# Kernel tuning notes

Measured on AMD Instinct MI355X. Metric: run time of the kernel, lower is better.

## Reference

```python
import math
import jax, jax.numpy as jnp
import numpy as np

B, S, D, QK, H = 4, 4096, 1024, 128, 2048  # hidden = int(2.0 * dim)
NUM_BUCKETS, MAX_DIST = 32, 128
LN_EPS = 1e-5


def setup_inputs() -> dict:
    key = jax.random.key(0)
    ks = jax.random.split(key, 7)
    x = jax.random.normal(ks[0], (B, S, D), jnp.float32)
    ln_g = jnp.ones((D,), jnp.float32)
    ln_b = jnp.zeros((D,), jnp.float32)
    Wh = jax.random.normal(ks[1], (D, 2 * H), jnp.float32) * 0.02
    bh = jnp.zeros((2 * H,), jnp.float32)
    Wqk = jax.random.normal(ks[2], (D, QK), jnp.float32) * 0.02
    bqk = jnp.zeros((QK,), jnp.float32)
    os_gamma = jax.random.normal(ks[3], (2, QK), jnp.float32) * 0.02  # nn.init.normal_(std=0.02)
    os_beta = jnp.zeros((2, QK), jnp.float32)
    Wo = jax.random.normal(ks[4], (H, D), jnp.float32) * 0.02
    bo = jnp.zeros((D,), jnp.float32)
    rel_emb = jax.random.normal(ks[5], (NUM_BUCKETS, 1), jnp.float32) * 0.02
    return {"x": x, "ln_g": ln_g, "ln_b": ln_b, "Wh": Wh, "bh": bh,
            "Wqk": Wqk, "bqk": bqk, "os_gamma": os_gamma, "os_beta": os_beta,
            "Wo": Wo, "bo": bo, "rel_emb": rel_emb}


def _t5_rel_bias(rel_emb, seq_len, scale):
    # non-causal T5 relative position bucket (num_buckets halved to 16)
    pos = jnp.arange(seq_len)
    rel = pos[None, :] - pos[:, None]  # k_pos - q_pos -> [i, j]
    n = -rel
    nb = NUM_BUCKETS // 2  # 16
    me = nb // 2           # max_exact = 8
    ret = (n < 0).astype(jnp.int32) * nb
    na = jnp.abs(n)
    val_large = me + (jnp.log(jnp.maximum(na, 1).astype(jnp.float32) / me)
                      / math.log(MAX_DIST / me) * (nb - me)).astype(jnp.int32)
    val_large = jnp.minimum(val_large, nb - 1)
    bucket = ret + jnp.where(na < me, na, val_large)  # [S, S] in [0, 31]
    return rel_emb[bucket, 0] * scale  # [S, S]


def reference(x, ln_g, ln_b, Wh, bh, Wqk, bqk, os_gamma, os_beta, Wo, bo, rel_emb):
    seq_len = x.shape[-2]
    # LayerNorm
    mu = jnp.mean(x, axis=-1, keepdims=True)
    var = jnp.mean(jnp.square(x - mu), axis=-1, keepdims=True)
    normed = (x - mu) * jax.lax.rsqrt(var + LN_EPS) * ln_g + ln_b
    # hidden (v, gate) with SiLU
    hidden = jax.nn.silu(normed @ Wh + bh)  # [B, S, 2H]
    v, gate = hidden[..., :H], hidden[..., H:]
    # qk projection + offset/scale into q, k
    qk = jax.nn.silu(normed @ Wqk + bqk)  # [B, S, QK]
    q = qk * os_gamma[0] + os_beta[0]
    k = qk * os_gamma[1] + os_beta[1]
    sim = jnp.einsum('bid,bjd->bij', q, k)  # [B, S, S]
    sim = sim + _t5_rel_bias(rel_emb, seq_len, float(D) ** 0.5)
    attn = jnp.square(jax.nn.relu(sim / seq_len))  # ReLU^2, no softmax
    out = jnp.einsum('bij,bjd->bid', attn, v) * gate  # [B, S, H]
    out = out @ Wo + bo
    return out + x  # add_residual
```

## Files before the change

kernel.cpp:

```cpp
#include <hip/hip_runtime.h>
#include <hip/hip_bf16.h>
#include <math.h>

typedef __bf16 bf16_t;
typedef __bf16 bf16x8 __attribute__((ext_vector_type(8)));
typedef __bf16 bf16x4 __attribute__((ext_vector_type(4)));
typedef float  f32x4  __attribute__((ext_vector_type(4)));
typedef int    i32x4  __attribute__((ext_vector_type(4)));

#define S_LEN 4096
#define D_DIM 1024
#define QK_DIM 128
#define H_DIM 2048
#define BATCH 4

__device__ __forceinline__ void gld_lds16(const void* g, void* l) {
  __builtin_amdgcn_global_load_lds((const __attribute__((address_space(1))) void*)g,
                                   (__attribute__((address_space(3))) void*)l, 16, 0, 0);
}

__device__ __forceinline__ float silu_f(float v) {
  return v / (1.0f + __expf(-v));
}

__device__ __forceinline__ bf16x8 as_bf(i32x4 v) {
  union { i32x4 a; bf16x8 b; } u; u.a = v; return u.b;
}

__device__ __forceinline__ float ldf(const void* p, size_t i, int f32) {
  return f32 ? ((const float*)p)[i] : (float)((const bf16_t*)p)[i];
}

__global__ void probe_k(const unsigned* __restrict__ ln_g_raw, int* __restrict__ flag) {
  if (threadIdx.x == 0) flag[0] = (ln_g_raw[0] == 0x3F800000u) ? 1 : 0;
}

#define M_HID 0
#define M_QK 1
#define M_SCORE 2
#define M_PV 3
#define M_OUT 4

template <int MODE, int K, int WAVES>
__global__ __launch_bounds__(WAVES * 64, 4)
void gemm2b(const bf16_t* __restrict__ A, const bf16_t* __restrict__ Bt,
            const void* e0, const void* e1, const float* __restrict__ ef,
            void* o0, void* o1, const int* __restrict__ dflag)
{
  constexpr int THREADS = WAVES * 64;
  constexpr int BN  = (WAVES == 8) ? 256 : 128;
  constexpr int NR  = 4;
  constexpr int ASLOT = 8192;
  constexpr int BSLOT = BN * 64;
  constexpr int NT  = K / 32;
  constexpr int RA  = ASLOT / (THREADS * 16);
  constexpr int RB  = BSLOT / (THREADS * 16);
  constexpr int SLD = RA + RB;

  __shared__ __align__(16) char lds[3 * (ASLOT + BSLOT)];

  const int t = threadIdx.x;
  const int w = t >> 6, lane = t & 63;
  const int quad = lane >> 4, col = lane & 15;
  const int wm = (WAVES == 8) ? ((w >> 2) * 64) : ((w >> 1) * 64);
  const int wn = (WAVES == 8) ? ((w & 3) * 64) : ((w & 1) * 64);

  const int gx = gridDim.x;
  const int nwg = gx * (int)gridDim.y;
  const int orig = (int)blockIdx.y * gx + (int)blockIdx.x;
  const int wg = (orig & 7) * (nwg >> 3) + (orig >> 3);
  const int bx = wg & (gx - 1), by = wg >> __builtin_ctz(gx);
  const int m0 = bx * 128, n0 = by * BN;

  const bf16_t* const Ap = A + (size_t)m0 * K;
  const bf16_t* const Bp = Bt + (size_t)n0 * K;

  size_t aoff[RA], boff[RB];
#pragma unroll
  for (int c = 0; c < RA; ++c) {
    const int P = c * THREADS * 16 + t * 16;
    const int L = P ^ (((P >> 7) & 3) << 4);
    aoff[c] = (size_t)(L >> 6) * K + ((L & 63) >> 1);
  }
#pragma unroll
  for (int c = 0; c < RB; ++c) {
    const int P = c * THREADS * 16 + t * 16;
    const int L = P ^ (((P >> 7) & 3) << 4);
    boff[c] = (size_t)(L >> 6) * K + ((L & 63) >> 1);
  }

  const int xr = (quad ^ ((col >> 1) & 3)) << 4;
  const unsigned ldsI = (unsigned)(size_t)&lds[0];
  const unsigned aStat = ldsI + (unsigned)((wm + col) * 64 + xr);
  const unsigned bStat = ldsI + 3u * ASLOT + (unsigned)((wn + col) * 64 + xr);

  f32x4 acc[4][NR] = {};
  i32x4 aF[4], bF[NR];

#define SB() __builtin_amdgcn_sched_barrier(0)
#define BARR() do { SB(); __builtin_amdgcn_s_barrier(); SB(); } while (0)
#define DSR(dst, addr, lit) \
  asm volatile("ds_read_b128 %0, %1 offset:" #lit : "=v"(dst) : "v"(addr))
#define WAITL0() asm volatile("s_waitcnt lgkmcnt(0)" ::: "memory")
#define WAITV0() asm volatile("s_waitcnt vmcnt(0)" ::: "memory")
#define VWS() do {                                                             \
    if constexpr (SLD == 3) asm volatile("s_waitcnt vmcnt(3)" ::: "memory");   \
    else                    asm volatile("s_waitcnt vmcnt(4)" ::: "memory");   \
  } while (0)

#define RD() do {                                                              \
    const unsigned aAd = aStat + (unsigned)(bsel * ASLOT);                     \
    const unsigned bAd = bStat + (unsigned)(bsel * BSLOT);                     \
    DSR(aF[0], aAd, 0);    DSR(aF[1], aAd, 1024);                              \
    DSR(aF[2], aAd, 2048); DSR(aF[3], aAd, 3072);                              \
    DSR(bF[0], bAd, 0);    DSR(bF[1], bAd, 1024);                              \
    DSR(bF[2], bAd, 2048); DSR(bF[3], bAd, 3072);                              \
  } while (0)

#define MM() do {                                                              \
    __builtin_amdgcn_s_setprio(1);                                             \
    _Pragma("unroll") for (int mi = 0; mi < 4; ++mi)                           \
    _Pragma("unroll") for (int ni = 0; ni < NR; ++ni)                          \
      acc[mi][ni] = __builtin_amdgcn_mfma_f32_16x16x32_bf16(                   \
          as_bf(aF[mi]), as_bf(bF[ni]), acc[mi][ni], 0, 0, 0);                 \
    __builtin_amdgcn_s_setprio(0);                                             \
  } while (0)

#define STG(ts, sl) do {                                                       \
    char* da_ = (char*)lds + (sl) * ASLOT + t * 16;                            \
    char* db_ = (char*)lds + 3 * ASLOT + (sl) * BSLOT + t * 16;                \
    const bf16_t* ga_ = Ap + (size_t)(ts) * 32;                                \
    const bf16_t* gb_ = Bp + (size_t)(ts) * 32;                                \
    _Pragma("unroll") for (int c_ = 0; c_ < RA; ++c_)                          \
      gld_lds16(ga_ + aoff[c_], da_ + c_ * THREADS * 16);                      \
    _Pragma("unroll") for (int c_ = 0; c_ < RB; ++c_)                          \
      gld_lds16(gb_ + boff[c_], db_ + c_ * THREADS * 16);                      \
  } while (0)

  STG(0, 0);
  STG(1, 1);
  VWS();
  BARR();

  int bsel = 0, ssel = 2;
  for (int tt = 0; tt < NT; ++tt) {
    RD();
    if (tt + 2 < NT) STG(tt + 2, ssel);
    WAITL0(); SB();
    MM();
    SB();
    if (tt + 1 < NT) {
      if (tt + 2 < NT) VWS();
      else WAITV0();
    }
    BARR();
    bsel = (bsel == 2) ? 0 : bsel + 1;
    ssel = (ssel == 2) ? 0 : ssel + 1;
  }

#undef SB
#undef BARR
#undef DSR
#undef WAITL0
#undef WAITV0
#undef VWS
#undef RD
#undef MM
#undef STG

  __syncthreads();

  int f32 = 0;
  if constexpr (MODE == M_HID || MODE == M_OUT) f32 = dflag[0];

  if constexpr (MODE == M_OUT) {
    float (*swzf)[16][68] = (float (*)[16][68])lds;
#pragma unroll
    for (int m = 0; m < 4; ++m) {
      __syncthreads();
#pragma unroll
      for (int j = 0; j < 4; ++j)
#pragma unroll
        for (int r = 0; r < 4; ++r)
          swzf[w][quad * 4 + r][j * 16 + col] = acc[m][j][r];
      __syncthreads();
#pragma unroll
      for (int it = 0; it < 4; ++it) {
        const int task = it * 64 + lane, gr = task >> 4, ch = task & 15;
        const int gm = m0 + wm + m * 16 + gr;
        const int gnc = n0 + wn + ch * 4;
        f32x4 vv = *(const f32x4*)&swzf[w][gr][ch * 4];
        float xr4[4], r4[4];
        if (f32) {
          float4 t4 = *(const float4*)((const float*)e1 + (size_t)gm * D_DIM + gnc);
          xr4[0] = t4.x; xr4[1] = t4.y; xr4[2] = t4.z; xr4[3] = t4.w;
        } else {
          bf16x4 t4 = *(const bf16x4*)((const bf16_t*)e1 + (size_t)gm * D_DIM + gnc);
#pragma unroll
          for (int qq = 0; qq < 4; ++qq) xr4[qq] = (float)t4[qq];
        }
#pragma unroll
        for (int qq = 0; qq < 4; ++qq)
          r4[qq] = vv[qq] + ldf(e0, gnc + qq, f32) + xr4[qq];
        if (f32) {
          float4 s4 = {r4[0], r4[1], r4[2], r4[3]};
          *(float4*)((float*)o0 + (size_t)gm * D_DIM + gnc) = s4;
        } else {
          bf16x4 s4;
#pragma unroll
          for (int qq = 0; qq < 4; ++qq) s4[qq] = (bf16_t)r4[qq];
          *(bf16x4*)((bf16_t*)o0 + (size_t)gm * D_DIM + gnc) = s4;
        }
      }
    }
    return;
  }

  if constexpr (MODE == M_HID) {
    if (n0 < H_DIM) {
      bf16_t (*swzT)[16][72] = (bf16_t (*)[16][72])lds;
      const int bb  = m0 >> 12;
      const int smb = (m0 + wm) & (S_LEN - 1);
#pragma unroll
      for (int j = 0; j < 4; ++j) {
        __syncthreads();
        const int gnj = n0 + wn + j * 16;
        const float bhv = ldf(e0, gnj + col, f32);
#pragma unroll
        for (int m = 0; m < 4; ++m)
#pragma unroll
          for (int r = 0; r < 4; ++r)
            swzT[w][col][m * 16 + quad * 4 + r] = (bf16_t)silu_f(acc[m][j][r] + bhv);
        __syncthreads();
#pragma unroll
        for (int it = 0; it < 2; ++it) {
          const int task = it * 64 + lane, gr = task >> 3, ch = task & 7;
          bf16x8 vv = *(const bf16x8*)&swzT[w][gr][ch * 8];
          const size_t off = ((size_t)bb * H_DIM + (gnj + gr)) * S_LEN + smb + ch * 8;
          *(bf16x8*)((bf16_t*)o0 + off) = vv;
        }
      }
      return;
    }
  }

  if constexpr (MODE == M_HID || MODE == M_SCORE || MODE == M_PV) {
    bf16_t (*swzb)[16][72] = (bf16_t (*)[16][72])lds;
#pragma unroll
    for (int m = 0; m < 4; ++m) {
      __syncthreads();
#pragma unroll
      for (int j = 0; j < 4; ++j) {
        const int gn = n0 + wn + j * 16 + col;
#pragma unroll
        for (int r = 0; r < 4; ++r) {
          const float val = acc[m][j][r];
          bf16_t sv;
          if constexpr (MODE == M_HID) {
            sv = (bf16_t)silu_f(val + ldf(e0, gn, f32));
          } else if constexpr (MODE == M_SCORE) {
            const int gm = m0 + wm + m * 16 + quad * 4 + r;
            float wgt = fmaxf((val + ef[gm - gn + (S_LEN - 1)]) *
                              (1.0f / (float)S_LEN), 0.0f);
            sv = (bf16_t)(wgt * wgt);
          } else {
            sv = (bf16_t)val;
          }
          swzb[w][quad * 4 + r][j * 16 + col] = sv;
        }
      }
      __syncthreads();
#pragma unroll
      for (int it = 0; it < 2; ++it) {
        const int task = it * 64 + lane, gr = task >> 3, ch = task & 7;
        const int gm  = m0 + wm + m * 16 + gr;
        const int gnb = n0 + wn + ch * 8;
        bf16x8 vv = *(const bf16x8*)&swzb[w][gr][ch * 8];
        if constexpr (MODE == M_HID) {
          *(bf16x8*)((bf16_t*)o1 + (size_t)gm * H_DIM + (gnb - H_DIM)) = vv;
        } else if constexpr (MODE == M_SCORE) {
          *(bf16x8*)((bf16_t*)o0 + (size_t)gm * S_LEN + gnb) = vv;
        } else {
          bf16x8 g8 = *(const bf16x8*)((const bf16_t*)e0 + (size_t)gm * H_DIM + gnb);
          bf16x8 r8;
#pragma unroll
          for (int qq = 0; qq < 8; ++qq)
            r8[qq] = (bf16_t)((float)vv[qq] * (float)g8[qq]);
          *(bf16x8*)((bf16_t*)o0 + (size_t)gm * H_DIM + gnb) = r8;
        }
      }
    }
  }
}

template <int MODE>
__global__ __launch_bounds__(256)
void gemm_bt(const bf16_t* __restrict__ A, const bf16_t* __restrict__ Bt,
             int M, int N, int K,
             const void* e0, const void* e1, const void* e2,
             const float* __restrict__ ef,
             void* o0, void* o1, const int* __restrict__ dflag)
{
  __shared__ __align__(16) bf16_t As[128 * 32];
  __shared__ __align__(16) bf16_t Bs[128 * 32];
  const int t = threadIdx.x;
  const int w = t >> 6, lane = t & 63;
  const int quad = lane >> 4, col = lane & 15;
  const int wm = (w >> 1) << 6, wn = (w & 1) << 6;
  const int m0 = blockIdx.x * 128, n0 = blockIdx.y * 128;
  const int f32 = dflag[0];

  f32x4 acc[4][4] = {};

  for (int k0 = 0; k0 < K; k0 += 32) {
    __syncthreads();
    for (int p = 0; p < 2; ++p) {
      const int chunk = w * 2 + p;
      const int fl = (chunk * 64 + lane) * 8;
      const int r = fl >> 5, c = fl & 31;
      gld_lds16(A  + (size_t)(m0 + r) * K + (k0 + c), &As[chunk * 512]);
      gld_lds16(Bt + (size_t)(n0 + r) * K + (k0 + c), &Bs[chunk * 512]);
    }
    __syncthreads();

    bf16x8 af[4], bfr[4];
#pragma unroll
    for (int i = 0; i < 4; ++i)
      af[i] = *(const bf16x8*)&As[(wm + i * 16 + col) * 32 + quad * 8];
#pragma unroll
    for (int i = 0; i < 4; ++i)
      bfr[i] = *(const bf16x8*)&Bs[(wn + i * 16 + col) * 32 + quad * 8];
#pragma unroll
    for (int i = 0; i < 4; ++i)
#pragma unroll
      for (int j = 0; j < 4; ++j)
        acc[i][j] = __builtin_amdgcn_mfma_f32_16x16x32_bf16(af[i], bfr[j], acc[i][j], 0, 0, 0);
  }

#pragma unroll
  for (int i = 0; i < 4; ++i) {
#pragma unroll
    for (int j = 0; j < 4; ++j) {
#pragma unroll
      for (int r = 0; r < 4; ++r) {
        const int gm = m0 + wm + i * 16 + quad * 4 + r;
        const int gn = n0 + wn + j * 16 + col;
        float val = acc[i][j][r] + ldf(e0, gn, f32);
        float s = silu_f(val);
        ((bf16_t*)o0)[(size_t)gm * QK_DIM + gn] =
            (bf16_t)(s * ldf(e1, gn, f32) + ldf(e2, gn, f32));
        ((bf16_t*)o1)[(size_t)gm * QK_DIM + gn] =
            (bf16_t)(s * ldf(e1, QK_DIM + gn, f32) + ldf(e2, QK_DIM + gn, f32));
      }
    }
  }
}

__global__ __launch_bounds__(256)
void layernorm_k(const void* __restrict__ x, const void* __restrict__ g,
                 const void* __restrict__ be, bf16_t* __restrict__ out,
                 const int* __restrict__ dflag)
{
  const int row = blockIdx.x;
  const int t = threadIdx.x;
  const int f32 = dflag[0];
  float f[4];
  if (f32) {
    const float* xr = (const float*)x + (size_t)row * D_DIM;
    float4 xv = *(const float4*)&xr[t * 4];
    f[0] = xv.x; f[1] = xv.y; f[2] = xv.z; f[3] = xv.w;
  } else {
    const bf16_t* xr = (const bf16_t*)x + (size_t)row * D_DIM;
    bf16x4 xv = *(const bf16x4*)&xr[t * 4];
#pragma unroll
    for (int i = 0; i < 4; ++i) f[i] = (float)xv[i];
  }
  float s = 0.f, sq = 0.f;
#pragma unroll
  for (int i = 0; i < 4; ++i) { s += f[i]; sq += f[i] * f[i]; }
#pragma unroll
  for (int off = 32; off > 0; off >>= 1) {
    s += __shfl_down(s, off);
    sq += __shfl_down(sq, off);
  }
  __shared__ float red[8];
  const int w = t >> 6;
  if ((t & 63) == 0) { red[w] = s; red[4 + w] = sq; }
  __syncthreads();
  s = red[0] + red[1] + red[2] + red[3];
  sq = red[4] + red[5] + red[6] + red[7];
  const float mu = s * (1.0f / D_DIM);
  const float var = sq * (1.0f / D_DIM) - mu * mu;
  const float inv = rsqrtf(var + 1e-5f);
  bf16x4 ov;
#pragma unroll
  for (int i = 0; i < 4; ++i) {
    float nv = (f[i] - mu) * inv * ldf(g, t * 4 + i, f32) + ldf(be, t * 4 + i, f32);
    ov[i] = (bf16_t)nv;
  }
  *(bf16x4*)&out[(size_t)row * D_DIM + t * 4] = ov;
}

__global__ __launch_bounds__(256)
void transpose_k(const void* __restrict__ src, bf16_t* __restrict__ dst,
                 int R, int C, const int* __restrict__ dflag)
{
  __shared__ bf16_t tile[32][33];
  const int f32 = dflag[0];
  const int c0 = blockIdx.x * 32, r0 = blockIdx.y * 32;
  for (int i = threadIdx.y; i < 32; i += 8)
    tile[i][threadIdx.x] = (bf16_t)ldf(src, (size_t)(r0 + i) * C + (c0 + threadIdx.x), f32);
  __syncthreads();
  for (int i = threadIdx.y; i < 32; i += 8)
    dst[(size_t)(c0 + i) * R + (r0 + threadIdx.x)] = tile[threadIdx.x][i];
}

__global__ void bias_k(const void* __restrict__ rel_emb, float* __restrict__ bias,
                       const int* __restrict__ dflag)
{
  int d = blockIdx.x * 256 + threadIdx.x;
  if (d >= 2 * S_LEN - 1) return;
  const int f32 = dflag[0];
  int n = d - (S_LEN - 1);
  int ret = (n < 0) ? 16 : 0;
  int na = n < 0 ? -n : n;
  int b;
  if (na < 8) b = na;
  else {
    float vl = logf((float)na * (1.0f / 8.0f)) / logf(16.0f) * 8.0f;
    int vi = 8 + (int)vl;
    b = vi > 15 ? 15 : vi;
  }
  bias[d] = ldf(rel_emb, ret + b, f32) * 32.0f;
}

extern "C" void kernel_launch(void* const* d_in, const int* in_sizes, int n_in,
                              void* d_out, int out_size, void* d_ws, size_t ws_size,
                              hipStream_t stream)
{
  const void* x    = d_in[0];
  const void* ln_g = d_in[1];
  const void* ln_b = d_in[2];
  const void* Wh   = d_in[3];
  const void* bh   = d_in[4];
  const void* Wqk  = d_in[5];
  const void* bqk  = d_in[6];
  const void* osg  = d_in[7];
  const void* osb  = d_in[8];
  const void* Wo   = d_in[9];
  const void* bo   = d_in[10];
  const void* rel  = d_in[11];

  const int BS = BATCH * S_LEN;
  char* p = (char*)d_ws;
  int*    flags  = (int*)p;     p += 256;
  float*  bias   = (float*)p;   p += (size_t)8192 * 4;
  bf16_t* WhT    = (bf16_t*)p;  p += (size_t)4096 * 1024 * 2;
  bf16_t* WqkT   = (bf16_t*)p;  p += (size_t)128 * 1024 * 2;
  bf16_t* WoT    = (bf16_t*)p;  p += (size_t)1024 * 2048 * 2;
  bf16_t* q      = (bf16_t*)p;  p += (size_t)BS * QK_DIM * 2;
  bf16_t* kk     = (bf16_t*)p;  p += (size_t)BS * QK_DIM * 2;
  bf16_t* vT     = (bf16_t*)p;  p += (size_t)BS * H_DIM * 2;
  bf16_t* gate   = (bf16_t*)p;  p += (size_t)BS * H_DIM * 2;
  bf16_t* normed = (bf16_t*)p;  p += (size_t)BS * D_DIM * 2;
  bf16_t* attn   = normed;
  bf16_t* pvg    = gate;

  probe_k<<<1, 64, 0, stream>>>((const unsigned*)ln_g, flags);
  bias_k<<<32, 256, 0, stream>>>(rel, bias, flags);
  transpose_k<<<dim3(4096 / 32, 1024 / 32), dim3(32, 8), 0, stream>>>(Wh, WhT, 1024, 4096, flags);
  transpose_k<<<dim3(128 / 32, 1024 / 32), dim3(32, 8), 0, stream>>>(Wqk, WqkT, 1024, 128, flags);
  transpose_k<<<dim3(1024 / 32, 2048 / 32), dim3(32, 8), 0, stream>>>(Wo, WoT, 2048, 1024, flags);
  layernorm_k<<<BS, 256, 0, stream>>>(x, ln_g, ln_b, normed, flags);

  gemm2b<M_HID, 1024, 8><<<dim3(BS / 128, 4096 / 256), 512, 0, stream>>>(
      normed, WhT, bh, nullptr, nullptr, vT, gate, flags);
  gemm_bt<M_QK><<<dim3(BS / 128, 1), 256, 0, stream>>>(
      normed, WqkT, BS, QK_DIM, 1024, bqk, osg, osb, nullptr, q, kk, flags);

  for (int b = 0; b < BATCH; ++b) {
    gemm2b<M_SCORE, QK_DIM, 8><<<dim3(S_LEN / 128, S_LEN / 256), 512, 0, stream>>>(
        q + (size_t)b * S_LEN * QK_DIM, kk + (size_t)b * S_LEN * QK_DIM,
        nullptr, nullptr, bias, attn, nullptr, flags);
    gemm2b<M_PV, S_LEN, 4><<<dim3(S_LEN / 128, H_DIM / 128), 256, 0, stream>>>(
        attn, vT + (size_t)b * S_LEN * H_DIM,
        gate + (size_t)b * S_LEN * H_DIM, nullptr, nullptr,
        pvg + (size_t)b * S_LEN * H_DIM, nullptr, flags);
  }

  gemm2b<M_OUT, H_DIM, 4><<<dim3(BS / 128, 1024 / 128), 256, 0, stream>>>(
      pvg, WoT, bo, x, nullptr, d_out, nullptr, flags);
}
```

Measured before the change: 901.3 us.

## Generalize GEMM to 8-wave BN=256 tiles with optional BM=256 for large GEMMs

Replaces the WAVES-templated GEMM with a BM-templated kernel that always uses 512 threads and 256-wide N tiles. It adds a 256x256 tile option, with 8 A-fragments per wave, for the hidden and output projections. The PV GEMM moves from 4-wave 128x128 tiles to 8-wave 128x256 tiles. Larger tiles raise operand reuse per LDS byte, at the cost of more registers, lower occupancy (launch bound of 2 blocks for BM=256) and fewer workgroups for the output GEMM.

```diff
diff --git a/kernel.cpp b/kernel.cpp
--- a/kernel.cpp
+++ b/kernel.cpp
@@ -41,50 +41,47 @@
 #define M_PV 3
 #define M_OUT 4
 
-template <int MODE, int K, int WAVES>
-__global__ __launch_bounds__(WAVES * 64, 4)
-void gemm2b(const bf16_t* __restrict__ A, const bf16_t* __restrict__ Bt,
-            const void* e0, const void* e1, const float* __restrict__ ef,
-            void* o0, void* o1, const int* __restrict__ dflag)
-{
-  constexpr int THREADS = WAVES * 64;
-  constexpr int BN  = (WAVES == 8) ? 256 : 128;
-  constexpr int NR  = 4;
-  constexpr int ASLOT = 8192;
-  constexpr int BSLOT = BN * 64;
+template <int MODE, int K, int BM>
+__global__ __launch_bounds__(512, (BM == 256 ? 2 : 4))
+void gemm3(const bf16_t* __restrict__ A, const bf16_t* __restrict__ Bt,
+           const void* e0, const void* e1, const float* __restrict__ ef,
+           void* o0, void* o1, const int* __restrict__ dflag)
+{
+  constexpr int MR  = BM / 32;
+  constexpr int ASLOT = BM * 64;
+  constexpr int BSLOT = 16384;
   constexpr int NT  = K / 32;
-  constexpr int RA  = ASLOT / (THREADS * 16);
-  constexpr int RB  = BSLOT / (THREADS * 16);
-  constexpr int SLD = RA + RB;
+  constexpr int RA  = BM / 128;
+  constexpr int SLD = RA + 2;
 
   __shared__ __align__(16) char lds[3 * (ASLOT + BSLOT)];
 
   const int t = threadIdx.x;
   const int w = t >> 6, lane = t & 63;
   const int quad = lane >> 4, col = lane & 15;
-  const int wm = (WAVES == 8) ? ((w >> 2) * 64) : ((w >> 1) * 64);
-  const int wn = (WAVES == 8) ? ((w & 3) * 64) : ((w & 1) * 64);
+  const int wm = (w >> 2) * (BM / 2);
+  const int wn = (w & 3) * 64;
 
   const int gx = gridDim.x;
   const int nwg = gx * (int)gridDim.y;
   const int orig = (int)blockIdx.y * gx + (int)blockIdx.x;
   const int wg = (orig & 7) * (nwg >> 3) + (orig >> 3);
   const int bx = wg & (gx - 1), by = wg >> __builtin_ctz(gx);
-  const int m0 = bx * 128, n0 = by * BN;
+  const int m0 = bx * BM, n0 = by * 256;
 
   const bf16_t* const Ap = A + (size_t)m0 * K;
   const bf16_t* const Bp = Bt + (size_t)n0 * K;
 
-  size_t aoff[RA], boff[RB];
+  size_t aoff[RA], boff[2];
 #pragma unroll
   for (int c = 0; c < RA; ++c) {
-    const int P = c * THREADS * 16 + t * 16;
+    const int P = c * 8192 + t * 16;
     const int L = P ^ (((P >> 7) & 3) << 4);
     aoff[c] = (size_t)(L >> 6) * K + ((L & 63) >> 1);
   }
 #pragma unroll
-  for (int c = 0; c < RB; ++c) {
-    const int P = c * THREADS * 16 + t * 16;
+  for (int c = 0; c < 2; ++c) {
+    const int P = c * 8192 + t * 16;
     const int L = P ^ (((P >> 7) & 3) << 4);
     boff[c] = (size_t)(L >> 6) * K + ((L & 63) >> 1);
   }
@@ -94,8 +91,8 @@
   const unsigned aStat = ldsI + (unsigned)((wm + col) * 64 + xr);
   const unsigned bStat = ldsI + 3u * ASLOT + (unsigned)((wn + col) * 64 + xr);
 
-  f32x4 acc[4][NR] = {};
-  i32x4 aF[4], bF[NR];
+  f32x4 acc[MR][4] = {};
+  i32x4 aF[MR], bF[4];
 
 #define SB() __builtin_amdgcn_sched_barrier(0)
 #define BARR() do { SB(); __builtin_amdgcn_s_barrier(); SB(); } while (0)
@@ -113,14 +110,18 @@
     const unsigned bAd = bStat + (unsigned)(bsel * BSLOT);                     \
     DSR(aF[0], aAd, 0);    DSR(aF[1], aAd, 1024);                              \
     DSR(aF[2], aAd, 2048); DSR(aF[3], aAd, 3072);                              \
+    if constexpr (MR == 8) {                                                   \
+      DSR(aF[4], aAd, 4096); DSR(aF[5], aAd, 5120);                            \
+      DSR(aF[6], aAd, 6144); DSR(aF[7], aAd, 7168);                            \
+    }                                                                          \
     DSR(bF[0], bAd, 0);    DSR(bF[1], bAd, 1024);                              \
     DSR(bF[2], bAd, 2048); DSR(bF[3], bAd, 3072);                              \
   } while (0)
 
 #define MM() do {                                                              \
     __builtin_amdgcn_s_setprio(1);                                             \
-    _Pragma("unroll") for (int mi = 0; mi < 4; ++mi)                           \
-    _Pragma("unroll") for (int ni = 0; ni < NR; ++ni)                          \
+    _Pragma("unroll") for (int mi = 0; mi < MR; ++mi)                          \
+    _Pragma("unroll") for (int ni = 0; ni < 4; ++ni)                           \
       acc[mi][ni] = __builtin_amdgcn_mfma_f32_16x16x32_bf16(                   \
           as_bf(aF[mi]), as_bf(bF[ni]), acc[mi][ni], 0, 0, 0);                 \
     __builtin_amdgcn_s_setprio(0);                                             \
@@ -132,9 +133,9 @@
     const bf16_t* ga_ = Ap + (size_t)(ts) * 32;                                \
     const bf16_t* gb_ = Bp + (size_t)(ts) * 32;                                \
     _Pragma("unroll") for (int c_ = 0; c_ < RA; ++c_)                          \
-      gld_lds16(ga_ + aoff[c_], da_ + c_ * THREADS * 16);                      \
-    _Pragma("unroll") for (int c_ = 0; c_ < RB; ++c_)                          \
-      gld_lds16(gb_ + boff[c_], db_ + c_ * THREADS * 16);                      \
+      gld_lds16(ga_ + aoff[c_], da_ + c_ * 8192);                              \
+    _Pragma("unroll") for (int c_ = 0; c_ < 2; ++c_)                           \
+      gld_lds16(gb_ + boff[c_], db_ + c_ * 8192);                              \
   } while (0)
 
   STG(0, 0);
@@ -176,7 +177,7 @@
   if constexpr (MODE == M_OUT) {
     float (*swzf)[16][68] = (float (*)[16][68])lds;
 #pragma unroll
-    for (int m = 0; m < 4; ++m) {
+    for (int m = 0; m < MR; ++m) {
       __syncthreads();
 #pragma unroll
       for (int j = 0; j < 4; ++j)
@@ -218,7 +219,8 @@
 
   if constexpr (MODE == M_HID) {
     if (n0 < H_DIM) {
-      bf16_t (*swzT)[16][72] = (bf16_t (*)[16][72])lds;
+      constexpr int TW = MR * 16 + 8;
+      bf16_t (*swzT)[16][TW] = (bf16_t (*)[16][TW])lds;
       const int bb  = m0 >> 12;
       const int smb = (m0 + wm) & (S_LEN - 1);
 #pragma unroll
@@ -227,14 +229,15 @@
         const int gnj = n0 + wn + j * 16;
         const float bhv = ldf(e0, gnj + col, f32);
 #pragma unroll
-        for (int m = 0; m < 4; ++m)
+        for (int m = 0; m < MR; ++m)
 #pragma unroll
           for (int r = 0; r < 4; ++r)
             swzT[w][col][m * 16 + quad * 4 + r] = (bf16_t)silu_f(acc[m][j][r] + bhv);
         __syncthreads();
 #pragma unroll
-        for (int it = 0; it < 2; ++it) {
-          const int task = it * 64 + lane, gr = task >> 3, ch = task & 7;
+        for (int it = 0; it < MR / 2; ++it) {
+          const int task = it * 64 + lane;
+          const int gr = task / (MR * 2), ch = task & (MR * 2 - 1);
           bf16x8 vv = *(const bf16x8*)&swzT[w][gr][ch * 8];
           const size_t off = ((size_t)bb * H_DIM + (gnj + gr)) * S_LEN + smb + ch * 8;
           *(bf16x8*)((bf16_t*)o0 + off) = vv;
@@ -247,7 +250,7 @@
   if constexpr (MODE == M_HID || MODE == M_SCORE || MODE == M_PV) {
     bf16_t (*swzb)[16][72] = (bf16_t (*)[16][72])lds;
 #pragma unroll
-    for (int m = 0; m < 4; ++m) {
+    for (int m = 0; m < MR; ++m) {
       __syncthreads();
 #pragma unroll
       for (int j = 0; j < 4; ++j) {
@@ -473,21 +476,21 @@
   transpose_k<<<dim3(1024 / 32, 2048 / 32), dim3(32, 8), 0, stream>>>(Wo, WoT, 2048, 1024, flags);
   layernorm_k<<<BS, 256, 0, stream>>>(x, ln_g, ln_b, normed, flags);
 
-  gemm2b<M_HID, 1024, 8><<<dim3(BS / 128, 4096 / 256), 512, 0, stream>>>(
+  gemm3<M_HID, 1024, 256><<<dim3(BS / 256, 4096 / 256), 512, 0, stream>>>(
       normed, WhT, bh, nullptr, nullptr, vT, gate, flags);
   gemm_bt<M_QK><<<dim3(BS / 128, 1), 256, 0, stream>>>(
       normed, WqkT, BS, QK_DIM, 1024, bqk, osg, osb, nullptr, q, kk, flags);
 
   for (int b = 0; b < BATCH; ++b) {
-    gemm2b<M_SCORE, QK_DIM, 8><<<dim3(S_LEN / 128, S_LEN / 256), 512, 0, stream>>>(
+    gemm3<M_SCORE, QK_DIM, 128><<<dim3(S_LEN / 128, S_LEN / 256), 512, 0, stream>>>(
         q + (size_t)b * S_LEN * QK_DIM, kk + (size_t)b * S_LEN * QK_DIM,
         nullptr, nullptr, bias, attn, nullptr, flags);
-    gemm2b<M_PV, S_LEN, 4><<<dim3(S_LEN / 128, H_DIM / 128), 256, 0, stream>>>(
+    gemm3<M_PV, S_LEN, 128><<<dim3(S_LEN / 128, H_DIM / 256), 512, 0, stream>>>(
         attn, vT + (size_t)b * S_LEN * H_DIM,
         gate + (size_t)b * S_LEN * H_DIM, nullptr, nullptr,
         pvg + (size_t)b * S_LEN * H_DIM, nullptr, flags);
   }
 
-  gemm2b<M_OUT, H_DIM, 4><<<dim3(BS / 128, 1024 / 128), 256, 0, stream>>>(
+  gemm3<M_OUT, H_DIM, 256><<<dim3(BS / 256, 1024 / 256), 512, 0, stream>>>(
       pvg, WoT, bo, x, nullptr, d_out, nullptr, flags);
 }
```

Result: faster. 818.2 us (-9.2%).
